# Kernel optimization log

Measured on AMD Instinct MI355X. Metric: run time of the kernel, lower is better.

## Reference

```python
import jax, jax.numpy as jnp
import numpy as np

RES_UP_RATIO = 0.05   # reserve_up_ratio (mgr.args default)
RES_DN_RATIO = 0.02   # reserve_dn_ratio
REQ_UP_RATIO = 0.02   # system_reserve_up_ratio
REQ_DN_RATIO = 0.02   # system_reserve_dn_ratio


def _build_K(G):
    """Static constraint matrix of the per-timestep LP over x=[P, R_up, R_dn] (n=3G).
    Row 0 is the equality sum(P)=D; remaining rows are <= inequalities."""
    n = 3 * G
    m = 1 + 4 * G + 2
    K = np.zeros((m, n), dtype=np.float32)
    I = np.eye(G, dtype=np.float32)
    K[0, :G] = 1.0                      # sum_g P = D
    r = 1
    K[r:r+G, :G] = I;  K[r:r+G, G:2*G] = I;  r += G      # P + R_up <= pmax
    K[r:r+G, :G] = -I; K[r:r+G, 2*G:3*G] = I; r += G     # -P + R_dn <= -pmin
    K[r:r+G, :G] = I;  r += G                             # P <= pmax
    K[r:r+G, :G] = -I; r += G                             # -P <= -pmin
    K[r, G:2*G] = -1.0; r += 1                            # -sum R_up <= -req_up*D
    K[r, 2*G:3*G] = -1.0                                  # -sum R_dn <= -req_dn*D
    return K


def _solve_da_lp(forecast, pmin, pmax, b, n_iters):
    """Batched PDHG (Chambolle-Pock) solve of all B*T per-timestep LPs.
    Returns P, R_up, R_dn with shape (B, T, G)."""
    B, T = forecast.shape
    G = b.shape[0]
    Knp = _build_K(G)
    L = float(np.linalg.norm(Knp, 2))          # static spectral norm of K
    tau = sigma = 0.9 / L
    K = jnp.asarray(Knp)
    m, n = K.shape
    # objective coefficients over x=[P, R_up, R_dn] (Cost = b*P + c is affine)
    c_obj = jnp.concatenate([b, RES_UP_RATIO * b, RES_DN_RATIO * b])  # (n,)
    # rhs q: (B, T, m)
    q = jnp.concatenate([
        forecast[..., None],
        jnp.broadcast_to(pmax, (B, T, G)),
        jnp.broadcast_to(-pmin, (B, T, G)),
        jnp.broadcast_to(pmax, (B, T, G)),
        jnp.broadcast_to(-pmin, (B, T, G)),
        -REQ_UP_RATIO * forecast[..., None],
        -REQ_DN_RATIO * forecast[..., None],
    ], axis=-1)
    ineq = (jnp.arange(m) > 0)  # row 0 = equality dual (unprojected)

    x0 = jnp.zeros((B, T, n), dtype=forecast.dtype)
    y0 = jnp.zeros((B, T, m), dtype=forecast.dtype)

    def step(carry, _):
        x, y = carry
        x_new = jnp.maximum(x - tau * (c_obj + jnp.einsum('btm,mn->btn', y, K)), 0.0)
        x_bar = 2.0 * x_new - x
        y_new = y + sigma * (jnp.einsum('btn,mn->btm', x_bar, K) - q)
        y_new = jnp.where(ineq, jnp.maximum(y_new, 0.0), y_new)
        return (x_new, y_new), None

    (x, _), _ = jax.lax.scan(step, (x0, y0), None, length=n_iters)
    P = x[..., :G]
    Ru = x[..., G:2*G]
    Rd = x[..., 2*G:3*G]
    return P, Ru, Rd


def setup_inputs() -> dict:
    key = jax.random.key(0)
    k1, k2, k3, k4 = jax.random.split(key, 4)
    G, B, T = 50, 128, 24
    pmax = 100.0 + 400.0 * jax.random.uniform(k1, (G,), dtype=jnp.float32)
    pmin = 0.1 * pmax
    b = 20.0 + 30.0 * jax.random.uniform(k2, (G,), dtype=jnp.float32)
    c = 100.0 * jax.random.uniform(k3, (G,), dtype=jnp.float32)
    lo, hi = jnp.sum(pmin), jnp.sum(pmax)
    # feasible demand: comfortably inside [sum pmin, sum pmax] so reserves exist
    forecast = lo + (0.35 + 0.3 * jax.random.uniform(k4, (B, T), dtype=jnp.float32)) * (hi - lo)
    return {"forecast": forecast, "pmin": pmin, "pmax": pmax, "b": b, "c": c, "n_iters": 300}


def reference(forecast, pmin, pmax, b, c, n_iters):
    P, Ru, Rd = _solve_da_lp(forecast, pmin, pmax, b, n_iters)  # (B,T,G)
    # match torch layout (B, G, T)
    P_DA = jnp.swapaxes(P, 1, 2)
    R_up = jnp.swapaxes(Ru, 1, 2)
    R_dn = jnp.swapaxes(Rd, 1, 2)
    Cost_DA = b[None, :, None] * P_DA + c[None, :, None]
    ru_price = (RES_UP_RATIO * b)[None, :, None]
    rd_price = (RES_DN_RATIO * b)[None, :, None]
    obj = Cost_DA.sum((1, 2)) + (ru_price * R_up).sum((1, 2)) + (rd_price * R_dn).sum((1, 2))
    return (P_DA, R_up, R_dn, obj, Cost_DA)
```

## Files before the change

### kernel.cpp

```cpp
#include <hip/hip_runtime.h>
#include <math.h>

#define G   50
#define T   24
#define B   128
#define NLP (B * T)
#define SZ  (B * G * T)

typedef float v2f __attribute__((ext_vector_type(2)));


__device__ __forceinline__ v2f vmax0(v2f v) {
    v2f z = {0.f, 0.f};
    return __builtin_elementwise_max(v, z);
}

template <int CTRL>
__device__ __forceinline__ float dpp_mov(float x) {
    int r = __builtin_amdgcn_update_dpp(0, __float_as_int(x), CTRL, 0xf, 0xf, true);
    return __int_as_float(r);
}

__device__ __forceinline__ void row_sum3(float& a, float& b, float& c) {
    asm("s_nop 1\n\t"
        "v_add_f32_dpp %0, %0, %0 row_ror:1 row_mask:0xf bank_mask:0xf\n\t"
        "v_add_f32_dpp %1, %1, %1 row_ror:1 row_mask:0xf bank_mask:0xf\n\t"
        "v_add_f32_dpp %2, %2, %2 row_ror:1 row_mask:0xf bank_mask:0xf\n\t"
        "v_add_f32_dpp %0, %0, %0 row_ror:2 row_mask:0xf bank_mask:0xf\n\t"
        "v_add_f32_dpp %1, %1, %1 row_ror:2 row_mask:0xf bank_mask:0xf\n\t"
        "v_add_f32_dpp %2, %2, %2 row_ror:2 row_mask:0xf bank_mask:0xf\n\t"
        "v_add_f32_dpp %0, %0, %0 row_ror:4 row_mask:0xf bank_mask:0xf\n\t"
        "v_add_f32_dpp %1, %1, %1 row_ror:4 row_mask:0xf bank_mask:0xf\n\t"
        "v_add_f32_dpp %2, %2, %2 row_ror:4 row_mask:0xf bank_mask:0xf\n\t"
        "v_add_f32_dpp %0, %0, %0 row_ror:8 row_mask:0xf bank_mask:0xf\n\t"
        "v_add_f32_dpp %1, %1, %1 row_ror:8 row_mask:0xf bank_mask:0xf\n\t"
        "v_add_f32_dpp %2, %2, %2 row_ror:8 row_mask:0xf bank_mask:0xf"
        : "+v"(a), "+v"(b), "+v"(c));
}

__device__ __forceinline__ float row_sum1(float a) {
    a += dpp_mov<0x121>(a);
    a += dpp_mov<0x122>(a);
    a += dpp_mov<0x124>(a);
    a += dpp_mov<0x128>(a);
    return a;
}

__global__ __launch_bounds__(64)
void pdhg_lp_kernel(const float* __restrict__ forecast,
                    const float* __restrict__ pmin,
                    const float* __restrict__ pmax,
                    const float* __restrict__ bcost,
                    const float* __restrict__ ccost,
                    const int*   __restrict__ n_iters_p,
                    float* __restrict__ out,
                    float* __restrict__ ws_partial,
                    float tau)
{
    const int lane = threadIdx.x;
    const int lh   = lane & 15;
    const int row  = lane >> 4;
    const int lp   = blockIdx.x * 4 + row;
    const int b    = lp / T;
    const int t    = lp - b * T;
    const int n_iters = n_iters_p[0];

    const int  gA0 = lh,      gA1 = lh + 16;
    const int  gB0 = lh + 32;
    const int  gB1 = lh + 48;
    const bool vB1 = (lh < 2);

    v2f bjA  = { bcost[gA0], bcost[gA1] };
    v2f bjB  = { bcost[gB0], vB1 ? bcost[gB1] : 0.f };
    v2f cjA  = { ccost[gA0], ccost[gA1] };
    v2f cjB  = { ccost[gB0], vB1 ? ccost[gB1] : 0.f };
    v2f pmxA = { pmax[gA0],  pmax[gA1] };
    v2f pmxB = { pmax[gB0],  vB1 ? pmax[gB1] : 0.f };
    v2f pmnA = { pmin[gA0],  pmin[gA1] };
    v2f pmnB = { pmin[gB0],  vB1 ? pmin[gB1] : 0.f };
    const float f = forecast[lp];

    const float ts  = tau * tau;
    const float BIG = 1e30f;

    v2f tcPA  = tau * bjA;
    v2f tcPB  = tau * bjB;           if (!vB1) tcPB.y  = BIG;
    v2f tcRuA = (tau * 0.05f) * bjA;
    v2f tcRuB = (tau * 0.05f) * bjB; if (!vB1) tcRuB.y = BIG;
    v2f tcRdA = (tau * 0.02f) * bjA;
    v2f tcRdB = (tau * 0.02f) * bjB; if (!vB1) tcRdB.y = BIG;
    v2f tspmxA = ts * pmxA, tspmxB = ts * pmxB;
    v2f tspmnA = ts * pmnA, tspmnB = ts * pmnB;
    const float tsf   = ts * f;
    const float tsreq = ts * 0.02f * f;

    v2f PA = {0,0}, PB = {0,0}, RuA = {0,0}, RuB = {0,0}, RdA = {0,0}, RdB = {0,0};
    v2f z1A = {0,0}, z1B = {0,0}, z2A = {0,0}, z2B = {0,0};
    v2f z3A = {0,0}, z3B = {0,0}, z4A = {0,0}, z4B = {0,0};
    float z0 = 0.f, zru = 0.f, zrd = 0.f;

    for (int it = 0; it < n_iters; ++it) {
        v2f z0v = { z0, z0 };
        v2f zruv = { zru, zru };
        v2f zrdv = { zrd, zrd };
        v2f gPA = (z1A - z2A) + (z3A - z4A) + z0v;
        v2f gPB = (z1B - z2B) + (z3B - z4B) + z0v;
        v2f PnA = vmax0(PA - tcPA - gPA);
        v2f PnB = vmax0(PB - tcPB - gPB);
        v2f RunA = vmax0(RuA - tcRuA - z1A + zruv);
        v2f RunB = vmax0(RuB - tcRuB - z1B + zruv);
        v2f RdnA = vmax0(RdA - tcRdA - z2A + zrdv);
        v2f RdnB = vmax0(RdB - tcRdB - z2B + zrdv);

        v2f PbA  = 2.f * PnA  - PA,  PbB  = 2.f * PnB  - PB;
        v2f RubA = 2.f * RunA - RuA, RubB = 2.f * RunB - RuB;
        v2f RdbA = 2.f * RdnA - RdA, RdbB = 2.f * RdnB - RdB;
        PA = PnA; PB = PnB; RuA = RunA; RuB = RunB; RdA = RdnA; RdB = RdnB;

        v2f tP = PbA + PbB, tRu = RubA + RubB, tRd = RdbA + RdbB;
        float sP  = tP.x  + tP.y;
        float sRu = tRu.x + tRu.y;
        float sRd = tRd.x + tRd.y;
        row_sum3(sP, sRu, sRd);

        z0  = z0 + ts * sP - tsf;
        z1A = vmax0(z1A + ts * (PbA + RubA) - tspmxA);
        z1B = vmax0(z1B + ts * (PbB + RubB) - tspmxB);
        z2A = vmax0(z2A + ts * (RdbA - PbA) + tspmnA);
        z2B = vmax0(z2B + ts * (RdbB - PbB) + tspmnB);
        z3A = vmax0(z3A + ts * PbA - tspmxA);
        z3B = vmax0(z3B + ts * PbB - tspmxB);
        z4A = vmax0(z4A - ts * PbA + tspmnA);
        z4B = vmax0(z4B - ts * PbB + tspmnB);
        zru = fmaxf(zru + tsreq - ts * sRu, 0.f);
        zrd = fmaxf(zrd + tsreq - ts * sRd, 0.f);
    }

    const v2f costA = bjA * PA + cjA;
    const v2f costB = bjB * PB + cjB;
    {
        const int bgt = b * (G * T) + t;
        const int a0 = bgt + gA0 * T, a1 = bgt + gA1 * T, b0 = bgt + gB0 * T;
        out[a0] = PA.x;  out[SZ + a0] = RuA.x;  out[2*SZ + a0] = RdA.x;  out[3*SZ + B + a0] = costA.x;
        out[a1] = PA.y;  out[SZ + a1] = RuA.y;  out[2*SZ + a1] = RdA.y;  out[3*SZ + B + a1] = costA.y;
        out[b0] = PB.x;  out[SZ + b0] = RuB.x;  out[2*SZ + b0] = RdB.x;  out[3*SZ + B + b0] = costB.x;
        if (vB1) {
            const int b1 = bgt + gB1 * T;
            out[b1] = PB.y;  out[SZ + b1] = RuB.y;  out[2*SZ + b1] = RdB.y;  out[3*SZ + B + b1] = costB.y;
        }
    }

    if (ws_partial) {
        v2f lo = costA + (0.05f * bjA) * RuA + (0.02f * bjA) * RdA
               + costB + (0.05f * bjB) * RuB + (0.02f * bjB) * RdB;
        float tot = row_sum1(lo.x + lo.y);
        if (lh == 0) ws_partial[lp] = tot;
    }
}

__global__ __launch_bounds__(64)
void obj_final_kernel(const float* __restrict__ ws_partial, float* __restrict__ out)
{
    const int b = blockIdx.x * 64 + threadIdx.x;
    if (b < B) {
        float s = 0.f;
        #pragma unroll
        for (int t = 0; t < T; ++t) s += ws_partial[b * T + t];
        out[3 * SZ + b] = s;
    }
}

__global__ __launch_bounds__(256)
void obj_kernel(const float* __restrict__ bcost, float* __restrict__ out)
{
    const int b = blockIdx.x;
    const float* Ru = out + SZ     + (size_t)b * (G * T);
    const float* Rd = out + 2 * SZ + (size_t)b * (G * T);
    const float* C  = out + 3 * SZ + B + (size_t)b * (G * T);

    float s = 0.f;
    for (int i = threadIdx.x; i < G * T; i += 256) {
        const int g = i / T;
        const float bg = bcost[g];
        s += C[i] + 0.05f * bg * Ru[i] + 0.02f * bg * Rd[i];
    }
    __shared__ float sm[16];
    s = row_sum1(s);
    if ((threadIdx.x & 15) == 0) sm[threadIdx.x >> 4] = s;
    __syncthreads();
    if (threadIdx.x == 0) {
        float tot = 0.f;
        #pragma unroll
        for (int i = 0; i < 16; ++i) tot += sm[i];
        out[3 * SZ + b] = tot;
    }
}

extern "C" void kernel_launch(void* const* d_in, const int* in_sizes, int n_in,
                              void* d_out, int out_size, void* d_ws, size_t ws_size,
                              hipStream_t stream) {
    const float* forecast = (const float*)d_in[0];
    const float* pmin_p   = (const float*)d_in[1];
    const float* pmax_p   = (const float*)d_in[2];
    const float* b_p      = (const float*)d_in[3];
    const float* c_p      = (const float*)d_in[4];
    const int*   niter_p  = (const int*)  d_in[5];
    float* out = (float*)d_out;

    const double L = sqrt((105.0 + sqrt(17.0)) * 0.5);
    const float tau = (float)(0.9 / L);

    const bool use_ws = (ws_size >= (size_t)NLP * sizeof(float));
    float* wsp = use_ws ? (float*)d_ws : nullptr;

    pdhg_lp_kernel<<<NLP / 4, 64, 0, stream>>>(forecast, pmin_p, pmax_p,
                                               b_p, c_p, niter_p, out, wsp, tau);
    if (use_ws) {
        obj_final_kernel<<<(B + 63) / 64, 64, 0, stream>>>(wsp, out);
    } else {
        obj_kernel<<<B, 256, 0, stream>>>(b_p, out);
    }
}
```

Before: 136.0 us.

## Map each LP to 32 lanes with scalar state and swizzle cross-row reduction

Changes the work split so each LP uses a 32-lane half-wave with two generators per lane, replacing the earlier 16-lane rows that each held four generators as packed v2f vectors. The per-lane serial chain of each PDHG iteration gets shorter and uses scalar fma and sign-flipped duals (fminf), at the cost of an extra ds_swizzle xor-16 step in every reduction. The launch doubles the number of blocks, which raises the wave count and parallelism but halves the LPs per wave. The swizzle goes through the LDS crossbar and may add latency to each iteration's reduction.

```diff
diff --git a/kernel.cpp b/kernel.cpp
--- a/kernel.cpp
+++ b/kernel.cpp
@@ -7,21 +7,8 @@
 #define NLP (B * T)
 #define SZ  (B * G * T)
 
-typedef float v2f __attribute__((ext_vector_type(2)));
-
-
-__device__ __forceinline__ v2f vmax0(v2f v) {
-    v2f z = {0.f, 0.f};
-    return __builtin_elementwise_max(v, z);
-}
-
-template <int CTRL>
-__device__ __forceinline__ float dpp_mov(float x) {
-    int r = __builtin_amdgcn_update_dpp(0, __float_as_int(x), CTRL, 0xf, 0xf, true);
-    return __int_as_float(r);
-}
-
-__device__ __forceinline__ void row_sum3(float& a, float& b, float& c) {
+
+__device__ __forceinline__ void rowror_sum3(float& a, float& b, float& c) {
     asm("s_nop 1\n\t"
         "v_add_f32_dpp %0, %0, %0 row_ror:1 row_mask:0xf bank_mask:0xf\n\t"
         "v_add_f32_dpp %1, %1, %1 row_ror:1 row_mask:0xf bank_mask:0xf\n\t"
@@ -38,6 +25,15 @@
         : "+v"(a), "+v"(b), "+v"(c));
 }
 
+__device__ __forceinline__ float swz_xor16(float x) {
+    return __int_as_float(__builtin_amdgcn_ds_swizzle(__float_as_int(x), 0x401F));
+}
+
+template <int CTRL>
+__device__ __forceinline__ float dpp_mov(float x) {
+    int r = __builtin_amdgcn_update_dpp(0, __float_as_int(x), CTRL, 0xf, 0xf, true);
+    return __int_as_float(r);
+}
 __device__ __forceinline__ float row_sum1(float a) {
     a += dpp_mov<0x121>(a);
     a += dpp_mov<0x122>(a);
@@ -58,103 +54,109 @@
                     float tau)
 {
     const int lane = threadIdx.x;
-    const int lh   = lane & 15;
-    const int row  = lane >> 4;
-    const int lp   = blockIdx.x * 4 + row;
+    const int lh   = lane & 31;
+    const int half = lane >> 5;
+    const int lp   = blockIdx.x * 2 + half;
     const int b    = lp / T;
     const int t    = lp - b * T;
     const int n_iters = n_iters_p[0];
 
-    const int  gA0 = lh,      gA1 = lh + 16;
-    const int  gB0 = lh + 32;
-    const int  gB1 = lh + 48;
-    const bool vB1 = (lh < 2);
-
-    v2f bjA  = { bcost[gA0], bcost[gA1] };
-    v2f bjB  = { bcost[gB0], vB1 ? bcost[gB1] : 0.f };
-    v2f cjA  = { ccost[gA0], ccost[gA1] };
-    v2f cjB  = { ccost[gB0], vB1 ? ccost[gB1] : 0.f };
-    v2f pmxA = { pmax[gA0],  pmax[gA1] };
-    v2f pmxB = { pmax[gB0],  vB1 ? pmax[gB1] : 0.f };
-    v2f pmnA = { pmin[gA0],  pmin[gA1] };
-    v2f pmnB = { pmin[gB0],  vB1 ? pmin[gB1] : 0.f };
-    const float f = forecast[lp];
+    const int  g0 = lh;
+    const int  g1 = lh + 32;
+    const bool v1 = (g1 < G);
+    const int  gl1 = v1 ? g1 : (G - 1);
+
+    const float bj0 = bcost[g0];
+    const float bj1 = v1 ? bcost[gl1] : 0.f;
+    const float cj0 = ccost[g0];
+    const float cj1 = v1 ? ccost[gl1] : 0.f;
+    const float f   = forecast[lp];
 
     const float ts  = tau * tau;
     const float BIG = 1e30f;
 
-    v2f tcPA  = tau * bjA;
-    v2f tcPB  = tau * bjB;           if (!vB1) tcPB.y  = BIG;
-    v2f tcRuA = (tau * 0.05f) * bjA;
-    v2f tcRuB = (tau * 0.05f) * bjB; if (!vB1) tcRuB.y = BIG;
-    v2f tcRdA = (tau * 0.02f) * bjA;
-    v2f tcRdB = (tau * 0.02f) * bjB; if (!vB1) tcRdB.y = BIG;
-    v2f tspmxA = ts * pmxA, tspmxB = ts * pmxB;
-    v2f tspmnA = ts * pmnA, tspmnB = ts * pmnB;
-    const float tsf   = ts * f;
-    const float tsreq = ts * 0.02f * f;
-
-    v2f PA = {0,0}, PB = {0,0}, RuA = {0,0}, RuB = {0,0}, RdA = {0,0}, RdB = {0,0};
-    v2f z1A = {0,0}, z1B = {0,0}, z2A = {0,0}, z2B = {0,0};
-    v2f z3A = {0,0}, z3B = {0,0}, z4A = {0,0}, z4B = {0,0};
+    const float tcP0   = tau * bj0;
+    const float tcP1   = v1 ? tau * bj1         : BIG;
+    const float tcRu0  = tau * 0.05f * bj0;
+    const float tcRu1  = v1 ? tau * 0.05f * bj1 : BIG;
+    const float tcRd0  = tau * 0.02f * bj0;
+    const float tcRd1  = v1 ? tau * 0.02f * bj1 : BIG;
+    const float tspmx0 = ts * pmax[g0];
+    const float tspmx1 = v1 ? ts * pmax[gl1] : 0.f;
+    const float tspmn0 = ts * pmin[g0];
+    const float tspmn1 = v1 ? ts * pmin[gl1] : 0.f;
+    const float tsf    = ts * f;
+    const float tsreq  = ts * 0.02f * f;
+
+    float P0 = 0.f, Ru0 = 0.f, Rd0 = 0.f, P1 = 0.f, Ru1 = 0.f, Rd1 = 0.f;
+    float z1_0 = 0.f, nz2_0 = 0.f, z3_0 = 0.f, nz4_0 = 0.f;
+    float z1_1 = 0.f, nz2_1 = 0.f, z3_1 = 0.f, nz4_1 = 0.f;
     float z0 = 0.f, zru = 0.f, zrd = 0.f;
 
     for (int it = 0; it < n_iters; ++it) {
-        v2f z0v = { z0, z0 };
-        v2f zruv = { zru, zru };
-        v2f zrdv = { zrd, zrd };
-        v2f gPA = (z1A - z2A) + (z3A - z4A) + z0v;
-        v2f gPB = (z1B - z2B) + (z3B - z4B) + z0v;
-        v2f PnA = vmax0(PA - tcPA - gPA);
-        v2f PnB = vmax0(PB - tcPB - gPB);
-        v2f RunA = vmax0(RuA - tcRuA - z1A + zruv);
-        v2f RunB = vmax0(RuB - tcRuB - z1B + zruv);
-        v2f RdnA = vmax0(RdA - tcRdA - z2A + zrdv);
-        v2f RdnB = vmax0(RdB - tcRdB - z2B + zrdv);
-
-        v2f PbA  = 2.f * PnA  - PA,  PbB  = 2.f * PnB  - PB;
-        v2f RubA = 2.f * RunA - RuA, RubB = 2.f * RunB - RuB;
-        v2f RdbA = 2.f * RdnA - RdA, RdbB = 2.f * RdnB - RdB;
-        PA = PnA; PB = PnB; RuA = RunA; RuB = RunB; RdA = RdnA; RdB = RdnB;
-
-        v2f tP = PbA + PbB, tRu = RubA + RubB, tRd = RdbA + RdbB;
-        float sP  = tP.x  + tP.y;
-        float sRu = tRu.x + tRu.y;
-        float sRd = tRd.x + tRd.y;
-        row_sum3(sP, sRu, sRd);
-
-        z0  = z0 + ts * sP - tsf;
-        z1A = vmax0(z1A + ts * (PbA + RubA) - tspmxA);
-        z1B = vmax0(z1B + ts * (PbB + RubB) - tspmxB);
-        z2A = vmax0(z2A + ts * (RdbA - PbA) + tspmnA);
-        z2B = vmax0(z2B + ts * (RdbB - PbB) + tspmnB);
-        z3A = vmax0(z3A + ts * PbA - tspmxA);
-        z3B = vmax0(z3B + ts * PbB - tspmxB);
-        z4A = vmax0(z4A - ts * PbA + tspmnA);
-        z4B = vmax0(z4B - ts * PbB + tspmnB);
-        zru = fmaxf(zru + tsreq - ts * sRu, 0.f);
-        zrd = fmaxf(zrd + tsreq - ts * sRd, 0.f);
-    }
-
-    const v2f costA = bjA * PA + cjA;
-    const v2f costB = bjB * PB + cjB;
+        float gP0 = ((z0 + z1_0) + (nz2_0 + z3_0)) + nz4_0;
+        float gP1 = ((z0 + z1_1) + (nz2_1 + z3_1)) + nz4_1;
+        float Pn0 = fmaxf(P0 - (tcP0 + gP0), 0.f);
+        float Pn1 = fmaxf(P1 - (tcP1 + gP1), 0.f);
+        float Run0 = fmaxf(((Ru0 - z1_0) + zru) - tcRu0, 0.f);
+        float Run1 = fmaxf(((Ru1 - z1_1) + zru) - tcRu1, 0.f);
+        float Rdn0 = fmaxf(((Rd0 + nz2_0) + zrd) - tcRd0, 0.f);
+        float Rdn1 = fmaxf(((Rd1 + nz2_1) + zrd) - tcRd1, 0.f);
+
+        float Pb0  = fmaf(2.f, Pn0,  -P0),  Pb1  = fmaf(2.f, Pn1,  -P1);
+        float Rub0 = fmaf(2.f, Run0, -Ru0), Rub1 = fmaf(2.f, Run1, -Ru1);
+        float Rdb0 = fmaf(2.f, Rdn0, -Rd0), Rdb1 = fmaf(2.f, Rdn1, -Rd1);
+        P0 = Pn0; P1 = Pn1; Ru0 = Run0; Ru1 = Run1; Rd0 = Rdn0; Rd1 = Rdn1;
+
+        float sP  = Pb0  + Pb1;
+        float sRu = Rub0 + Rub1;
+        float sRd = Rdb0 + Rdb1;
+        rowror_sum3(sP, sRu, sRd);
+        float wP  = swz_xor16(sP);
+        float wRu = swz_xor16(sRu);
+        float wRd = swz_xor16(sRd);
+
+        z1_0  = fmaxf(fmaf(ts, Pb0 + Rub0, z1_0)  - tspmx0, 0.f);
+        z1_1  = fmaxf(fmaf(ts, Pb1 + Rub1, z1_1)  - tspmx1, 0.f);
+        nz2_0 = fminf(fmaf(ts, Pb0 - Rdb0, nz2_0) - tspmn0, 0.f);
+        nz2_1 = fminf(fmaf(ts, Pb1 - Rdb1, nz2_1) - tspmn1, 0.f);
+        z3_0  = fmaxf(fmaf(ts, Pb0, z3_0)  - tspmx0, 0.f);
+        z3_1  = fmaxf(fmaf(ts, Pb1, z3_1)  - tspmx1, 0.f);
+        nz4_0 = fminf(fmaf(ts, Pb0, nz4_0) - tspmn0, 0.f);
+        nz4_1 = fminf(fmaf(ts, Pb1, nz4_1) - tspmn1, 0.f);
+
+        sP  += wP;
+        sRu += wRu;
+        sRd += wRd;
+        z0  = fmaf(ts, sP, z0) - tsf;
+        zru = fmaxf(fmaf(-ts, sRu, zru + tsreq), 0.f);
+        zrd = fmaxf(fmaf(-ts, sRd, zrd + tsreq), 0.f);
+    }
+
+    const float cost0 = bj0 * P0 + cj0;
+    const float cost1 = bj1 * P1 + cj1;
     {
         const int bgt = b * (G * T) + t;
-        const int a0 = bgt + gA0 * T, a1 = bgt + gA1 * T, b0 = bgt + gB0 * T;
-        out[a0] = PA.x;  out[SZ + a0] = RuA.x;  out[2*SZ + a0] = RdA.x;  out[3*SZ + B + a0] = costA.x;
-        out[a1] = PA.y;  out[SZ + a1] = RuA.y;  out[2*SZ + a1] = RdA.y;  out[3*SZ + B + a1] = costA.y;
-        out[b0] = PB.x;  out[SZ + b0] = RuB.x;  out[2*SZ + b0] = RdB.x;  out[3*SZ + B + b0] = costB.x;
-        if (vB1) {
-            const int b1 = bgt + gB1 * T;
-            out[b1] = PB.y;  out[SZ + b1] = RuB.y;  out[2*SZ + b1] = RdB.y;  out[3*SZ + B + b1] = costB.y;
+        const int i0 = bgt + g0 * T;
+        out[i0]              = P0;
+        out[SZ + i0]         = Ru0;
+        out[2 * SZ + i0]     = Rd0;
+        out[3 * SZ + B + i0] = cost0;
+        if (v1) {
+            const int i1 = bgt + g1 * T;
+            out[i1]              = P1;
+            out[SZ + i1]         = Ru1;
+            out[2 * SZ + i1]     = Rd1;
+            out[3 * SZ + B + i1] = cost1;
         }
     }
 
     if (ws_partial) {
-        v2f lo = costA + (0.05f * bjA) * RuA + (0.02f * bjA) * RdA
-               + costB + (0.05f * bjB) * RuB + (0.02f * bjB) * RdB;
-        float tot = row_sum1(lo.x + lo.y);
-        if (lh == 0) ws_partial[lp] = tot;
+        float lo = cost0 + 0.05f * bj0 * Ru0 + 0.02f * bj0 * Rd0
+                 + (v1 ? (cost1 + 0.05f * bj1 * Ru1 + 0.02f * bj1 * Rd1) : 0.f);
+        float s = row_sum1(lo);
+        s += swz_xor16(s);
+        if (lh == 0) ws_partial[lp] = s;
     }
 }
 
@@ -184,14 +186,15 @@
         const float bg = bcost[g];
         s += C[i] + 0.05f * bg * Ru[i] + 0.02f * bg * Rd[i];
     }
-    __shared__ float sm[16];
     s = row_sum1(s);
-    if ((threadIdx.x & 15) == 0) sm[threadIdx.x >> 4] = s;
+    s += swz_xor16(s);
+    __shared__ float sm[8];
+    if ((threadIdx.x & 31) == 0) sm[threadIdx.x >> 5] = s;
     __syncthreads();
     if (threadIdx.x == 0) {
         float tot = 0.f;
         #pragma unroll
-        for (int i = 0; i < 16; ++i) tot += sm[i];
+        for (int i = 0; i < 8; ++i) tot += sm[i];
         out[3 * SZ + b] = tot;
     }
 }
@@ -213,7 +216,7 @@
     const bool use_ws = (ws_size >= (size_t)NLP * sizeof(float));
     float* wsp = use_ws ? (float*)d_ws : nullptr;
 
-    pdhg_lp_kernel<<<NLP / 4, 64, 0, stream>>>(forecast, pmin_p, pmax_p,
+    pdhg_lp_kernel<<<NLP / 2, 64, 0, stream>>>(forecast, pmin_p, pmax_p,
                                                b_p, c_p, niter_p, out, wsp, tau);
     if (use_ws) {
         obj_final_kernel<<<(B + 63) / 64, 64, 0, stream>>>(wsp, out);
```

Result: slower. 158.0 us (+16.2%).
